# Performance work log

Measured on AMD Instinct MI355X. Metric: run time of the kernel, lower is better.

The kernel has to match this reference:

```python
import jax, jax.numpy as jnp
import numpy as np

TWO_PI = 2.0 * 3.14159  # matches the torch source constant exactly
N_RINGS = 5
N_ORIENT = 8


def setup_inputs() -> dict:
    key = jax.random.key(0)
    k1, k2, k3 = jax.random.split(key, 3)
    B, N, CIN, COUT = 4, 32768, 32, 32
    features = jax.random.normal(k1, (B, N, CIN), dtype=jnp.float32)
    # radial in [0,1), angular in [0, 2*pi)
    coords01 = jax.random.uniform(k2, (B, N, 2), dtype=jnp.float32)
    geodesic_coords = coords01 * jnp.array([1.0, TWO_PI], dtype=jnp.float32)
    filters = jax.random.normal(k3, (N_RINGS, N_ORIENT, CIN, COUT), dtype=jnp.float32) * 0.01
    bias = jnp.zeros((COUT,), dtype=jnp.float32)
    return {"features": features, "geodesic_coords": geodesic_coords,
            "filters": filters, "bias": bias}


def reference(features, geodesic_coords, filters, bias):
    radial = geodesic_coords[:, :, 0]
    angular = geodesic_coords[:, :, 1]
    # torch .long() truncates toward zero; values are non-negative so astype matches
    ring_idx = jnp.clip((radial * N_RINGS).astype(jnp.int32), 0, N_RINGS - 1)
    orient_idx = jnp.clip((angular * N_ORIENT / TWO_PI).astype(jnp.int32), 0, N_ORIENT - 1)
    # gather per-point filter matrix: (B, N, Cin, Cout)
    W = filters[ring_idx, orient_idx]
    out = jnp.einsum('bnc,bncd->bnd', features, W) + bias
    return out
```

## Files before the change

kernel.cpp:

```cpp
#include <hip/hip_runtime.h>


#define NBINS 40
#define NB_MAX 4
#define PTS_BLK 64
#define MAX_NBLK 128

__device__ __forceinline__ int bin_of(float2 rc) {
    const float TWO_PI_F = (float)(2.0 * 3.14159);
    int ri = (int)(rc.x * 5.0f);
    ri = min(max(ri, 0), 4);
    int oi = (int)((rc.y * 8.0f) / TWO_PI_F);
    oi = min(max(oi, 0), 7);
    return ri * 8 + oi;
}

__global__ __launch_bounds__(1024)
void k_hist(const float2* __restrict__ coords, int* __restrict__ hist,
            unsigned char* __restrict__ bins_u8, int npts) {
    __shared__ int h[NBINS];
    const int tid = threadIdx.x;
    if (tid < NBINS) h[tid] = 0;
    __syncthreads();
    const int p = blockIdx.x * 1024 + tid;
    if (p < npts) {
        const int b = bin_of(coords[p]);
        bins_u8[p] = (unsigned char)b;
        atomicAdd(&h[b], 1);
    }
    __syncthreads();
    if (tid < NBINS) hist[blockIdx.x * NBINS + tid] = h[tid];
}

__global__ __launch_bounds__(1024)
void k_scan(const int* __restrict__ hist, int* __restrict__ blkoff, int nblk) {
    __shared__ int lh[MAX_NBLK * NBINS];
    __shared__ int btot[NBINS];
    __shared__ int base[NBINS];
    const int tid  = threadIdx.x;
    const int wave = tid >> 6;
    const int lane = tid & 63;
    for (int i = tid; i < nblk * NBINS; i += 1024) lh[i] = hist[i];
    __syncthreads();
    for (int b = wave; b < NBINS; b += 16) {
        int v0 = lh[lane * NBINS + b];
        int v1 = lh[(64 + lane) * NBINS + b];
        #pragma unroll
        for (int off = 1; off < 64; off <<= 1) { int t = __shfl_up(v0, off); if (lane >= off) v0 += t; }
        const int tot0 = __shfl(v0, 63);
        #pragma unroll
        for (int off = 1; off < 64; off <<= 1) { int t = __shfl_up(v1, off); if (lane >= off) v1 += t; }
        const int total = __shfl(v1, 63) + tot0;
        int e0 = __shfl_up(v0, 1); if (lane == 0) e0 = 0;
        int e1 = __shfl_up(v1, 1); if (lane == 0) e1 = 0;
        e1 += tot0;
        lh[lane * NBINS + b] = e0;
        lh[(64 + lane) * NBINS + b] = e1;
        if (lane == 0) btot[b] = total;
    }
    __syncthreads();
    if (wave == 0) {
        int v = (lane < NBINS) ? btot[lane] : 0;
        #pragma unroll
        for (int off = 1; off < 64; off <<= 1) { int t = __shfl_up(v, off); if (lane >= off) v += t; }
        int e = __shfl_up(v, 1); if (lane == 0) e = 0;
        if (lane < NBINS) base[lane] = e;
    }
    __syncthreads();
    for (int i = tid; i < nblk * NBINS; i += 1024) {
        const int b = i - (i / NBINS) * NBINS;
        blkoff[i] = lh[i] + base[b];
    }
}

__global__ __launch_bounds__(1024)
void k_scatter(const unsigned char* __restrict__ bins_u8, const int* __restrict__ blkoff,
               int* __restrict__ sorted_pk, int npts) {
    __shared__ int off[NBINS];
    __shared__ int cnt[NBINS];
    const int tid = threadIdx.x;
    if (tid < NBINS) { off[tid] = blkoff[blockIdx.x * NBINS + tid]; cnt[tid] = 0; }
    __syncthreads();
    const int p = blockIdx.x * 1024 + tid;
    if (p < npts) {
        const int b = (int)bins_u8[p];
        const int r = atomicAdd(&cnt[b], 1);
        sorted_pk[off[b] + r] = p | (b << 20);
    }
}

#define GEMM_BODY(W4EXPR)                                                     \
    unsigned long long rem = __ballot(1);                                     \
    while (rem) {                                                             \
        const int src = (int)__ffsll((long long)rem) - 1;                     \
        const int bb  = __shfl(b, src);                                       \
        const unsigned long long m = __ballot(b == bb);                       \
        rem &= ~m;                                                            \
        const bool act = (b == bb);                                           \
        const float4* __restrict__ W4 = (W4EXPR);                             \
        _Pragma("unroll")                                                     \
        for (int c = 0; c < 32; ++c) {                                        \
            const float fc = act ? f[c] : 0.0f;                               \
            const float4 w0 = W4[c * 8 + q * 2 + 0];                          \
            const float4 w1 = W4[c * 8 + q * 2 + 1];                          \
            acc[0] = fmaf(fc, w0.x, acc[0]);                                  \
            acc[1] = fmaf(fc, w0.y, acc[1]);                                  \
            acc[2] = fmaf(fc, w0.z, acc[2]);                                  \
            acc[3] = fmaf(fc, w0.w, acc[3]);                                  \
            acc[4] = fmaf(fc, w1.x, acc[4]);                                  \
            acc[5] = fmaf(fc, w1.y, acc[5]);                                  \
            acc[6] = fmaf(fc, w1.z, acc[6]);                                  \
            acc[7] = fmaf(fc, w1.w, acc[7]);                                  \
        }                                                                     \
    }

__global__ __launch_bounds__(256, 4)
void k_gemm(const float* __restrict__ feat, const float* __restrict__ filt,
            const float* __restrict__ bias, const int* __restrict__ sorted_pk,
            float* __restrict__ out) {
    __shared__ float4 Wl[NB_MAX * 256];
    const int tid     = threadIdx.x;
    const int q       = tid & 3;
    const int pl      = tid >> 2;
    const int blkbase = blockIdx.x * PTS_BLK;

    const int pk  = sorted_pk[blkbase + pl];
    const int idx = pk & 0xFFFFF;
    const int b   = pk >> 20;

    const int b0 = sorted_pk[blkbase] >> 20;
    const int b1 = sorted_pk[blkbase + PTS_BLK - 1] >> 20;
    const int nb = b1 - b0 + 1;

    const float4* __restrict__ filt4 = reinterpret_cast<const float4*>(filt);
    if (nb <= NB_MAX) {
        for (int i = tid; i < nb * 256; i += 256) Wl[i] = filt4[b0 * 256 + i];
    }
    __syncthreads();

    const float4* fp = reinterpret_cast<const float4*>(feat + (size_t)idx * 32);
    float f[32];
    #pragma unroll
    for (int g = 0; g < 8; ++g) {
        const float4 v = fp[g];
        f[g * 4 + 0] = v.x; f[g * 4 + 1] = v.y; f[g * 4 + 2] = v.z; f[g * 4 + 3] = v.w;
    }

    float acc[8];
    {
        const float4* bp = reinterpret_cast<const float4*>(bias) + q * 2;
        const float4 bv0 = bp[0], bv1 = bp[1];
        acc[0] = bv0.x; acc[1] = bv0.y; acc[2] = bv0.z; acc[3] = bv0.w;
        acc[4] = bv1.x; acc[5] = bv1.y; acc[6] = bv1.z; acc[7] = bv1.w;
    }

    if (nb <= NB_MAX) {
        GEMM_BODY(&Wl[(bb - b0) * 256])
    } else {
        GEMM_BODY(&filt4[(size_t)bb * 256])
    }

    float4* op = reinterpret_cast<float4*>(out + (size_t)idx * 32 + q * 8);
    op[0] = make_float4(acc[0], acc[1], acc[2], acc[3]);
    op[1] = make_float4(acc[4], acc[5], acc[6], acc[7]);
}

extern "C" void kernel_launch(void* const* d_in, const int* in_sizes, int n_in,
                              void* d_out, int out_size, void* d_ws, size_t ws_size,
                              hipStream_t stream) {
    const float*  feat   = (const float*)d_in[0];
    const float2* coords = (const float2*)d_in[1];
    const float*  filt   = (const float*)d_in[2];
    const float*  bias   = (const float*)d_in[3];
    float* out = (float*)d_out;

    const int npts = in_sizes[0] / 32;
    const int nblk = (npts + 1023) / 1024;

    int* sorted_pk           = (int*)d_ws;
    int* hist                = sorted_pk + npts;
    int* blkoff              = hist + nblk * NBINS;
    unsigned char* bins_u8   = (unsigned char*)(blkoff + nblk * NBINS);

    k_hist   <<<nblk, 1024, 0, stream>>>(coords, hist, bins_u8, npts);
    k_scan   <<<1,    1024, 0, stream>>>(hist, blkoff, nblk);
    k_scatter<<<nblk, 1024, 0, stream>>>(bins_u8, blkoff, sorted_pk, npts);
    k_gemm   <<<npts / PTS_BLK, 256, 0, stream>>>(feat, filt, bias, sorted_pk, out);
}
```

Measured before the change: 88.24 us.

## Stage gathered features in swizzled LDS and compute two points per thread

Each GEMM block now handles 128 sorted points. Feature rows are gathered cooperatively into XOR-swizzled shared memory with coalesced float4 loads, and each thread computes 16 outputs covering two points. Every weight load from LDS is therefore reused for two points, and the per-thread strided row gathers are replaced. The cost is more shared memory and registers, a lower grid size, and a bin loop that may take more iterations when the two points fall in different bins.

```diff
diff --git a/kernel.cpp b/kernel.cpp
--- a/kernel.cpp
+++ b/kernel.cpp
@@ -3,7 +3,7 @@
 
 #define NBINS 40
 #define NB_MAX 4
-#define PTS_BLK 64
+#define PTS_BLK 128
 #define MAX_NBLK 128
 
 __device__ __forceinline__ int bin_of(float2 rc) {
@@ -89,28 +89,37 @@
     }
 }
 
-#define GEMM_BODY(W4EXPR)                                                     \
-    unsigned long long rem = __ballot(1);                                     \
-    while (rem) {                                                             \
-        const int src = (int)__ffsll((long long)rem) - 1;                     \
-        const int bb  = __shfl(b, src);                                       \
-        const unsigned long long m = __ballot(b == bb);                       \
-        rem &= ~m;                                                            \
-        const bool act = (b == bb);                                           \
-        const float4* __restrict__ W4 = (W4EXPR);                             \
+#define GEMM_PASS(W4BASE)                                                     \
+    _Pragma("unroll")                                                         \
+    for (int c4 = 0; c4 < 8; ++c4) {                                          \
+        const int sw = c4 ^ swz;                                              \
+        const float4 fA4 = Fl[pp * 8 + sw];                                   \
+        const float4 fB4 = Fl[(pp + 64) * 8 + sw];                            \
+        const float fA[4] = {aA ? fA4.x : 0.f, aA ? fA4.y : 0.f,              \
+                             aA ? fA4.z : 0.f, aA ? fA4.w : 0.f};             \
+        const float fB[4] = {aB ? fB4.x : 0.f, aB ? fB4.y : 0.f,              \
+                             aB ? fB4.z : 0.f, aB ? fB4.w : 0.f};             \
         _Pragma("unroll")                                                     \
-        for (int c = 0; c < 32; ++c) {                                        \
-            const float fc = act ? f[c] : 0.0f;                               \
-            const float4 w0 = W4[c * 8 + q * 2 + 0];                          \
-            const float4 w1 = W4[c * 8 + q * 2 + 1];                          \
-            acc[0] = fmaf(fc, w0.x, acc[0]);                                  \
-            acc[1] = fmaf(fc, w0.y, acc[1]);                                  \
-            acc[2] = fmaf(fc, w0.z, acc[2]);                                  \
-            acc[3] = fmaf(fc, w0.w, acc[3]);                                  \
-            acc[4] = fmaf(fc, w1.x, acc[4]);                                  \
-            acc[5] = fmaf(fc, w1.y, acc[5]);                                  \
-            acc[6] = fmaf(fc, w1.z, acc[6]);                                  \
-            acc[7] = fmaf(fc, w1.w, acc[7]);                                  \
+        for (int j = 0; j < 4; ++j) {                                         \
+            const int c = c4 * 4 + j;                                         \
+            const float4 w0 = (W4BASE)[c * 8 + q * 2 + 0];                    \
+            const float4 w1 = (W4BASE)[c * 8 + q * 2 + 1];                    \
+            acc[0]  = fmaf(fA[j], w0.x, acc[0]);                              \
+            acc[1]  = fmaf(fA[j], w0.y, acc[1]);                              \
+            acc[2]  = fmaf(fA[j], w0.z, acc[2]);                              \
+            acc[3]  = fmaf(fA[j], w0.w, acc[3]);                              \
+            acc[4]  = fmaf(fA[j], w1.x, acc[4]);                              \
+            acc[5]  = fmaf(fA[j], w1.y, acc[5]);                              \
+            acc[6]  = fmaf(fA[j], w1.z, acc[6]);                              \
+            acc[7]  = fmaf(fA[j], w1.w, acc[7]);                              \
+            acc[8]  = fmaf(fB[j], w0.x, acc[8]);                              \
+            acc[9]  = fmaf(fB[j], w0.y, acc[9]);                              \
+            acc[10] = fmaf(fB[j], w0.z, acc[10]);                             \
+            acc[11] = fmaf(fB[j], w0.w, acc[11]);                             \
+            acc[12] = fmaf(fB[j], w1.x, acc[12]);                             \
+            acc[13] = fmaf(fB[j], w1.y, acc[13]);                             \
+            acc[14] = fmaf(fB[j], w1.z, acc[14]);                             \
+            acc[15] = fmaf(fB[j], w1.w, acc[15]);                             \
         }                                                                     \
     }
 
@@ -119,50 +128,82 @@
             const float* __restrict__ bias, const int* __restrict__ sorted_pk,
             float* __restrict__ out) {
     __shared__ float4 Wl[NB_MAX * 256];
+    __shared__ float4 Fl[PTS_BLK * 8];
+    __shared__ int    Pidx[PTS_BLK];
+    __shared__ int    Pbin[PTS_BLK];
+
     const int tid     = threadIdx.x;
-    const int q       = tid & 3;
-    const int pl      = tid >> 2;
     const int blkbase = blockIdx.x * PTS_BLK;
 
-    const int pk  = sorted_pk[blkbase + pl];
-    const int idx = pk & 0xFFFFF;
-    const int b   = pk >> 20;
-
-    const int b0 = sorted_pk[blkbase] >> 20;
-    const int b1 = sorted_pk[blkbase + PTS_BLK - 1] >> 20;
+    if (tid < PTS_BLK) {
+        const int pk = sorted_pk[blkbase + tid];
+        Pidx[tid] = pk & 0xFFFFF;
+        Pbin[tid] = pk >> 20;
+    }
+    __syncthreads();
+
+    const int b0 = Pbin[0];
+    const int b1 = Pbin[PTS_BLK - 1];
     const int nb = b1 - b0 + 1;
 
     const float4* __restrict__ filt4 = reinterpret_cast<const float4*>(filt);
     if (nb <= NB_MAX) {
         for (int i = tid; i < nb * 256; i += 256) Wl[i] = filt4[b0 * 256 + i];
     }
-    __syncthreads();
-
-    const float4* fp = reinterpret_cast<const float4*>(feat + (size_t)idx * 32);
-    float f[32];
-    #pragma unroll
-    for (int g = 0; g < 8; ++g) {
-        const float4 v = fp[g];
-        f[g * 4 + 0] = v.x; f[g * 4 + 1] = v.y; f[g * 4 + 2] = v.z; f[g * 4 + 3] = v.w;
-    }
-
-    float acc[8];
+    {
+        const int r  = tid >> 3;
+        const int c4 = tid & 7;
+        #pragma unroll
+        for (int pass = 0; pass < 4; ++pass) {
+            const int row = pass * 32 + r;
+            const float4 v = reinterpret_cast<const float4*>(
+                                 feat + (size_t)Pidx[row] * 32)[c4];
+            Fl[row * 8 + (c4 ^ (row & 7))] = v;
+        }
+    }
+    __syncthreads();
+
+    const int q   = tid & 3;
+    const int pp  = tid >> 2;
+    const int swz = pp & 7;
+    const int bA  = Pbin[pp];
+    const int bB  = Pbin[pp + 64];
+
+    float acc[16];
     {
         const float4* bp = reinterpret_cast<const float4*>(bias) + q * 2;
         const float4 bv0 = bp[0], bv1 = bp[1];
-        acc[0] = bv0.x; acc[1] = bv0.y; acc[2] = bv0.z; acc[3] = bv0.w;
-        acc[4] = bv1.x; acc[5] = bv1.y; acc[6] = bv1.z; acc[7] = bv1.w;
-    }
-
-    if (nb <= NB_MAX) {
-        GEMM_BODY(&Wl[(bb - b0) * 256])
-    } else {
-        GEMM_BODY(&filt4[(size_t)bb * 256])
-    }
-
-    float4* op = reinterpret_cast<float4*>(out + (size_t)idx * 32 + q * 8);
-    op[0] = make_float4(acc[0], acc[1], acc[2], acc[3]);
-    op[1] = make_float4(acc[4], acc[5], acc[6], acc[7]);
+        acc[0] = bv0.x; acc[1] = bv0.y; acc[2]  = bv0.z; acc[3]  = bv0.w;
+        acc[4] = bv1.x; acc[5] = bv1.y; acc[6]  = bv1.z; acc[7]  = bv1.w;
+        acc[8] = bv0.x; acc[9] = bv0.y; acc[10] = bv0.z; acc[11] = bv0.w;
+        acc[12] = bv1.x; acc[13] = bv1.y; acc[14] = bv1.z; acc[15] = bv1.w;
+    }
+
+    bool dA = false, dB = false;
+    while (true) {
+        const int want = !dA ? bA : (!dB ? bB : -1);
+        const unsigned long long v = __ballot(want >= 0);
+        if (!v) break;
+        const int src = (int)__ffsll((long long)v) - 1;
+        const int bb  = __shfl(want, src);
+        const bool aA = (bA == bb);
+        const bool aB = (bB == bb);
+        if (nb <= NB_MAX) {
+            const float4* __restrict__ W4 = &Wl[(bb - b0) * 256];
+            GEMM_PASS(W4)
+        } else {
+            const float4* __restrict__ W4 = &filt4[(size_t)bb * 256];
+            GEMM_PASS(W4)
+        }
+        dA |= aA; dB |= aB;
+    }
+
+    float4* oA = reinterpret_cast<float4*>(out + (size_t)Pidx[pp] * 32 + q * 8);
+    oA[0] = make_float4(acc[0], acc[1], acc[2], acc[3]);
+    oA[1] = make_float4(acc[4], acc[5], acc[6], acc[7]);
+    float4* oB = reinterpret_cast<float4*>(out + (size_t)Pidx[pp + 64] * 32 + q * 8);
+    oB[0] = make_float4(acc[8], acc[9], acc[10], acc[11]);
+    oB[1] = make_float4(acc[12], acc[13], acc[14], acc[15]);
 }
 
 extern "C" void kernel_launch(void* const* d_in, const int* in_sizes, int n_in,
```

Measured after the change: 92.50 us. 1.05x slower.
